# Optimization experiments

Measured on AMD Instinct MI355X. Metric: run time of the kernel, lower is better.

The kernel has to match this reference:

```python
import jax, jax.numpy as jnp
import numpy as np


def setup_inputs() -> dict:
    key = jax.random.key(0)
    B, N = 256, 512
    # binary symmetric-ish adjacency (0/1 entries)
    adj = jax.random.randint(key, (B, N, N), 0, 2).astype(jnp.float32)
    return {"adjacency": adj}


def reference(adjacency):
    # atom mask: rows with any connection
    atom_mask = (jnp.sum(adjacency, axis=-1) != 0).astype(adjacency.dtype)  # [B, N]
    N = adjacency.shape[-1]
    eye = jnp.eye(N, dtype=adjacency.dtype)
    # set_diag(adjacency, atom_mask): zero existing diagonal, insert mask
    adjacency_hat = adjacency * (1.0 - eye) + eye * atom_mask[..., :, None]
    degree_hat = jnp.sum(adjacency_hat, axis=-1)  # [B, N]
    d_sqrt = jnp.sqrt(degree_hat)
    # reciprocal_no_nan: 1/x where x != 0, else 0
    d_inv_sqrt = jnp.where(d_sqrt == 0, 0.0, 1.0 / jnp.where(d_sqrt == 0, 1.0, d_sqrt))
    # D^-1/2 A_hat D^-1/2 as row/column scaling (equivalent to the diag matmuls)
    adjacency_norm = d_inv_sqrt[..., :, None] * adjacency_hat * d_inv_sqrt[..., None, :]
    return adjacency_norm
```

## Files before the change

kernel.cpp:

```cpp
#include <hip/hip_runtime.h>
#include <hip/hip_bf16.h>


#define NN 512
#define NB 256

typedef float f32x4 __attribute__((ext_vector_type(4)));

__global__ __launch_bounds__(1024) void fused_norm_kernel(
    const float* __restrict__ adj, float* __restrict__ out) {
    __shared__ float sdinv[NN];

    const int b = blockIdx.x;
    const size_t base4 = (size_t)b * (NN * (NN / 4));
    const f32x4* a4 = (const f32x4*)adj + base4;
    f32x4*       o4 = (f32x4*)out + base4;

    const int tid  = threadIdx.x;
    const int wave = tid >> 6;
    const int lane = tid & 63;

    for (int rr = 0; rr < 32; ++rr) {
        const int row = wave * 32 + rr;
        const f32x4* r4 = a4 + row * (NN / 4);
        f32x4 x0 = r4[lane];
        f32x4 x1 = r4[lane + 64];

        float s = (x0.x + x0.y) + (x0.z + x0.w) + (x1.x + x1.y) + (x1.z + x1.w);

        float diag = 0.0f;
        int j0 = lane << 2;
        if (row >= j0 && row < j0 + 4) diag = ((const float*)&x0)[row - j0];
        int j1 = 256 + (lane << 2);
        if (row >= j1 && row < j1 + 4) diag = ((const float*)&x1)[row - j1];

        #pragma unroll
        for (int off = 32; off > 0; off >>= 1) {
            s    += __shfl_xor(s, off);
            diag += __shfl_xor(diag, off);
        }
        if (lane == 0) {
            float mask = (s != 0.0f) ? 1.0f : 0.0f;
            float deg  = s - diag + mask;
            sdinv[row] = (deg > 0.0f) ? (1.0f / sqrtf(deg)) : 0.0f;
        }
    }
    __syncthreads();

    const int j4    = tid & 127;
    const int rbase = tid >> 7;
    const f32x4 dj = ((const f32x4*)sdinv)[j4];
    const int jj = j4 << 2;

    for (int it = 63; it >= 0; --it) {
        const int row = rbase + (it << 3);
        const float di = sdinv[row];
        const size_t k = (size_t)row * (NN / 4) + j4;
        f32x4 a = a4[k];
        f32x4 o;
        o.x = (di * ((jj + 0 == row) ? 1.0f : a.x)) * dj.x;
        o.y = (di * ((jj + 1 == row) ? 1.0f : a.y)) * dj.y;
        o.z = (di * ((jj + 2 == row) ? 1.0f : a.z)) * dj.z;
        o.w = (di * ((jj + 3 == row) ? 1.0f : a.w)) * dj.w;
        __builtin_nontemporal_store(o, &o4[k]);
    }
}

extern "C" void kernel_launch(void* const* d_in, const int* in_sizes, int n_in,
                              void* d_out, int out_size, void* d_ws, size_t ws_size,
                              hipStream_t stream) {
    const float* adj = (const float*)d_in[0];
    float* out = (float*)d_out;
    fused_norm_kernel<<<NB, 1024, 0, stream>>>(adj, out);
}
```

Before: 484.8 us.

## Split each batch across 8 cooperating blocks with LDS tile and global sync

Each block now owns a 64-row slice of 8 different batches and loads that slice once into a 128KB LDS tile. It computes the row degrees from the tile, publishes them to a global workspace, and waits on a per-batch atomic counter until all 8 slices are done. The output is then written from LDS, so the input is read from HBM only once instead of twice. In exchange it adds inter-block spin-waits that assume all 256 blocks are resident at once, plus an extra kernel launch to reset the counters.

```diff
diff --git a/kernel.cpp b/kernel.cpp
--- a/kernel.cpp
+++ b/kernel.cpp
@@ -2,67 +2,98 @@
 #include <hip/hip_bf16.h>
 
 
-#define NN 512
-#define NB 256
+#define NN   512
+#define NB   256
+#define SROWS 64
+#define TPB  1024
 
 typedef float f32x4 __attribute__((ext_vector_type(4)));
 
-__global__ __launch_bounds__(1024) void fused_norm_kernel(
-    const float* __restrict__ adj, float* __restrict__ out) {
+__global__ void init_counters(unsigned* __restrict__ c) {
+    c[threadIdx.x] = 0u;
+}
+
+__global__ __launch_bounds__(TPB) void fused_kernel(
+    const float* __restrict__ adj, float* __restrict__ out,
+    float* __restrict__ dinvg, unsigned* __restrict__ counters) {
+    __shared__ float tile[SROWS * NN];
     __shared__ float sdinv[NN];
-
-    const int b = blockIdx.x;
-    const size_t base4 = (size_t)b * (NN * (NN / 4));
-    const f32x4* a4 = (const f32x4*)adj + base4;
-    f32x4*       o4 = (f32x4*)out + base4;
 
     const int tid  = threadIdx.x;
     const int wave = tid >> 6;
     const int lane = tid & 63;
+    const int grp  = blockIdx.x >> 3;
+    const int s    = blockIdx.x & 7;
 
-    for (int rr = 0; rr < 32; ++rr) {
-        const int row = wave * 32 + rr;
-        const f32x4* r4 = a4 + row * (NN / 4);
-        f32x4 x0 = r4[lane];
-        f32x4 x1 = r4[lane + 64];
+    for (int r = 0; r < 8; ++r) {
+        const int b = r * 32 + grp;
+        const size_t sliceBase4 =
+            (size_t)b * (NN * NN / 4) + (size_t)s * (SROWS * NN / 4);
+        const f32x4* src4 = (const f32x4*)adj + sliceBase4;
 
-        float s = (x0.x + x0.y) + (x0.z + x0.w) + (x1.x + x1.y) + (x1.z + x1.w);
-
-        float diag = 0.0f;
-        int j0 = lane << 2;
-        if (row >= j0 && row < j0 + 4) diag = ((const float*)&x0)[row - j0];
-        int j1 = 256 + (lane << 2);
-        if (row >= j1 && row < j1 + 4) diag = ((const float*)&x1)[row - j1];
+        f32x4 v[8];
+        #pragma unroll
+        for (int i = 0; i < 8; ++i) v[i] = src4[i * TPB + tid];
+        #pragma unroll
+        for (int i = 0; i < 8; ++i) ((f32x4*)tile)[i * TPB + tid] = v[i];
+        __syncthreads();
 
         #pragma unroll
-        for (int off = 32; off > 0; off >>= 1) {
-            s    += __shfl_xor(s, off);
-            diag += __shfl_xor(diag, off);
+        for (int rr = 0; rr < 4; ++rr) {
+            const int lr = wave * 4 + rr;
+            const f32x4* row4 = (const f32x4*)(tile + lr * NN);
+            f32x4 x0 = row4[lane];
+            f32x4 x1 = row4[lane + 64];
+            float ssum = (x0.x + x0.y) + (x0.z + x0.w)
+                       + (x1.x + x1.y) + (x1.z + x1.w);
+            #pragma unroll
+            for (int off = 32; off > 0; off >>= 1) ssum += __shfl_xor(ssum, off);
+            if (lane == 0) {
+                const int gi = s * SROWS + lr;
+                float diag = tile[lr * NN + gi];
+                float mask = (ssum != 0.0f) ? 1.0f : 0.0f;
+                float deg  = ssum - diag + mask;
+                float di   = (deg > 0.0f) ? (1.0f / sqrtf(deg)) : 0.0f;
+                __hip_atomic_store(&dinvg[(size_t)b * NN + gi], di,
+                                   __ATOMIC_RELAXED, __HIP_MEMORY_SCOPE_AGENT);
+            }
         }
-        if (lane == 0) {
-            float mask = (s != 0.0f) ? 1.0f : 0.0f;
-            float deg  = s - diag + mask;
-            sdinv[row] = (deg > 0.0f) ? (1.0f / sqrtf(deg)) : 0.0f;
+        __syncthreads();
+
+        if (tid == 0) {
+            __hip_atomic_fetch_add(&counters[b], 1u,
+                                   __ATOMIC_RELEASE, __HIP_MEMORY_SCOPE_AGENT);
+            while (__hip_atomic_load(&counters[b], __ATOMIC_ACQUIRE,
+                                     __HIP_MEMORY_SCOPE_AGENT) < 8u)
+                __builtin_amdgcn_s_sleep(2);
         }
-    }
-    __syncthreads();
+        __syncthreads();
 
-    const int j4    = tid & 127;
-    const int rbase = tid >> 7;
-    const f32x4 dj = ((const f32x4*)sdinv)[j4];
-    const int jj = j4 << 2;
+        if (tid < NN)
+            sdinv[tid] = __hip_atomic_load(&dinvg[(size_t)b * NN + tid],
+                                           __ATOMIC_RELAXED,
+                                           __HIP_MEMORY_SCOPE_AGENT);
+        __syncthreads();
 
-    for (int it = 63; it >= 0; --it) {
-        const int row = rbase + (it << 3);
-        const float di = sdinv[row];
-        const size_t k = (size_t)row * (NN / 4) + j4;
-        f32x4 a = a4[k];
-        f32x4 o;
-        o.x = (di * ((jj + 0 == row) ? 1.0f : a.x)) * dj.x;
-        o.y = (di * ((jj + 1 == row) ? 1.0f : a.y)) * dj.y;
-        o.z = (di * ((jj + 2 == row) ? 1.0f : a.z)) * dj.z;
-        o.w = (di * ((jj + 3 == row) ? 1.0f : a.w)) * dj.w;
-        __builtin_nontemporal_store(o, &o4[k]);
+        f32x4* dst4 = (f32x4*)out + sliceBase4;
+        #pragma unroll
+        for (int i = 0; i < 8; ++i) {
+            const int idx4  = i * TPB + tid;
+            const int row_l = idx4 >> 7;
+            const int c4    = idx4 & 127;
+            const int gi    = s * SROWS + row_l;
+            f32x4 a  = ((const f32x4*)tile)[idx4];
+            float di = sdinv[gi];
+            f32x4 dj = ((const f32x4*)sdinv)[c4];
+            const int j = c4 << 2;
+            f32x4 o;
+            o.x = (di * ((j + 0 == gi) ? 1.0f : a.x)) * dj.x;
+            o.y = (di * ((j + 1 == gi) ? 1.0f : a.y)) * dj.y;
+            o.z = (di * ((j + 2 == gi) ? 1.0f : a.z)) * dj.z;
+            o.w = (di * ((j + 3 == gi) ? 1.0f : a.w)) * dj.w;
+            __builtin_nontemporal_store(o, &dst4[idx4]);
+        }
+        __syncthreads();
     }
 }
 
@@ -71,5 +102,9 @@
                               hipStream_t stream) {
     const float* adj = (const float*)d_in[0];
     float* out = (float*)d_out;
-    fused_norm_kernel<<<NB, 1024, 0, stream>>>(adj, out);
+    unsigned* counters = (unsigned*)d_ws;
+    float* dinvg = (float*)((char*)d_ws + 4096);
+
+    init_counters<<<1, NB, 0, stream>>>(counters);
+    fused_kernel<<<NB, TPB, 0, stream>>>(adj, out, dinvg, counters);
 }
```

Result: slower. 535.3 us (+10.4%).
